# Kernel optimization log

Measured on AMD Instinct MI355X. Metric: run time of the kernel, lower is better.

## Reference

```python
import jax, jax.numpy as jnp
import numpy as np
from jax import lax

WS = 7          # window size
SHIFT = 3       # shift size
HEADS = 16
DIM = 512
NREF = 100
H_IMG = 112
W_IMG = 112
BATCH = 2
HD = DIM // HEADS
SCALE = HD ** (-0.5)
EPS = 1e-5


def _layernorm(x, w, b):
    mu = jnp.mean(x, axis=-1, keepdims=True)
    var = jnp.mean((x - mu) ** 2, axis=-1, keepdims=True)
    return (x - mu) / jnp.sqrt(var + EPS) * w + b


def _rel_pos_index():
    coords = np.stack(np.meshgrid(np.arange(WS), np.arange(WS), indexing='ij'))  # (2,ws,ws)
    cf = coords.reshape(2, -1)
    rel = cf[:, :, None] - cf[:, None, :]
    rel = rel.transpose(1, 2, 0).astype(np.int64)
    rel[..., 0] += WS - 1
    rel[..., 1] += WS - 1
    rel[..., 0] *= 2 * WS - 1
    return rel.sum(-1).reshape(-1)  # (N*N,)

_RPI = _rel_pos_index()


def setup_inputs() -> dict:
    key = jax.random.key(0)
    ks = jax.random.split(key, 16)
    C = DIM
    s = 0.02
    x = jax.random.normal(ks[0], (BATCH, H_IMG * W_IMG, C), jnp.float32)
    x_ref = jax.random.normal(ks[1], (BATCH, NREF, C), jnp.float32)
    # shifted-window attention mask (standard Swin construction)
    img = np.zeros((H_IMG, W_IMG))
    cnt = 0
    for hs in (slice(0, -WS), slice(-WS, -SHIFT), slice(-SHIFT, None)):
        for ws_ in (slice(0, -WS), slice(-WS, -SHIFT), slice(-SHIFT, None)):
            img[hs, ws_] = cnt
            cnt += 1
    mw = img.reshape(H_IMG // WS, WS, W_IMG // WS, WS).transpose(0, 2, 1, 3).reshape(-1, WS * WS)
    am = mw[:, None, :] - mw[:, :, None]
    mask = jnp.asarray(np.where(am != 0, -100.0, 0.0), jnp.float32)  # (nW, N, N)
    return dict(
        x=x, x_ref=x_ref, mask=mask,
        norm1_w=jnp.ones((C,), jnp.float32), norm1_b=jnp.zeros((C,), jnp.float32),
        qkv_w=jax.random.normal(ks[2], (3 * C, C), jnp.float32) * s,
        qkv_b=jnp.zeros((3 * C,), jnp.float32),
        diff_mu=jax.random.normal(ks[3], (1, 1, C), jnp.float32),
        diff_logsigma=jax.random.normal(ks[4], (1, 1, C), jnp.float32) * s,
        rpb_table=jax.random.normal(ks[5], ((2 * WS - 1) ** 2, HEADS), jnp.float32) * s,
        ref_qk_w=jax.random.normal(ks[6], (2 * C, C), jnp.float32) * s,
        ref_qk_b=jnp.zeros((2 * C,), jnp.float32),
        conv_w=jax.random.normal(ks[7], (HEADS, HEADS, 3, 3), jnp.float32) * s,
        conv_b=jnp.zeros((HEADS,), jnp.float32),
        proj_w=jax.random.normal(ks[8], (C, C), jnp.float32) * s,
        proj_b=jnp.zeros((C,), jnp.float32),
        norm2_w=jnp.ones((C,), jnp.float32), norm2_b=jnp.zeros((C,), jnp.float32),
        fc1_w=jax.random.normal(ks[9], (4 * C, C), jnp.float32) * s,
        fc1_b=jnp.zeros((4 * C,), jnp.float32),
        fc2_w=jax.random.normal(ks[10], (C, 4 * C), jnp.float32) * s,
        fc2_b=jnp.zeros((C,), jnp.float32),
        Hh=H_IMG, Ww=W_IMG,
    )


def _window_attention(xw, mask, x_ref, qkv_w, qkv_b, diff_mu, diff_logsigma,
                      rpb_table, ref_qk_w, ref_qk_b, conv_w, conv_b, proj_w, proj_b):
    B_, N, C = xw.shape
    rB = x_ref.shape[0]
    n_win = B_ // rB
    qkv = (xw @ qkv_w.T + qkv_b).reshape(B_, N, 3, HEADS, HD).transpose(2, 0, 3, 1, 4)
    q, k, v = qkv[0], qkv[1], qkv[2]  # (B_, heads, N, hd)
    # reference tokens -> q/v with reparameterized shift/scale
    ref_qk = (x_ref @ ref_qk_w.T + ref_qk_b).reshape(rB, NREF, 2, C).transpose(2, 0, 1, 3)
    ref_q = diff_mu + jnp.exp(diff_logsigma) * ref_qk[0]
    ref_q = ref_q.reshape(rB, NREF, HEADS, HD).transpose(0, 2, 1, 3)
    ref_v = ref_qk[1].reshape(rB, NREF, HEADS, HD).transpose(0, 2, 1, 3)
    ref_k = jnp.repeat(ref_q, n_win, axis=0)  # (B_, heads, nref, hd)
    ref_v = jnp.repeat(ref_v, n_win, axis=0)
    ra = jnp.einsum('bhnd,bhrd->bhnr', q, ref_k)  # (B_, heads, N, nref)
    ra = ra.reshape(rB, n_win, HEADS, N, NREF).transpose(0, 2, 1, 3, 4).reshape(rB, HEADS, n_win * N, NREF)
    # 3 rounds of conv diffusion + layernorm(no affine) + gelu, residual
    for _ in range(3):
        u = lax.conv_general_dilated(ra, conv_w, (1, 1), 'SAME',
                                     dimension_numbers=('NCHW', 'OIHW', 'NCHW'))
        u = u + conv_b[None, :, None, None]
        mu = jnp.mean(u, axis=(-2, -1), keepdims=True)
        var = jnp.mean((u - mu) ** 2, axis=(-2, -1), keepdims=True)
        u = jax.nn.gelu((u - mu) / jnp.sqrt(var + EPS), approximate=False)
        ra = ra + u
    ra = ra.reshape(rB, HEADS, n_win, N, NREF).transpose(0, 2, 1, 3, 4).reshape(B_, HEADS, N, NREF)
    ra = jax.nn.softmax(ra, axis=-1)
    q_new = jnp.einsum('bhnr,bhrd->bhnd', ra, ref_v) * SCALE
    attn = jnp.einsum('bhnd,bhmd->bhnm', q_new, k)
    rpb = rpb_table[_RPI].reshape(N, N, HEADS).transpose(2, 0, 1)  # (heads, N, N)
    attn = attn + rpb[None]
    nW = mask.shape[0]
    attn = attn.reshape(B_ // nW, nW, HEADS, N, N) + mask[None, :, None]
    attn = jax.nn.softmax(attn.reshape(B_, HEADS, N, N), axis=-1)
    out = jnp.einsum('bhnm,bhmd->bhnd', attn, v).transpose(0, 2, 1, 3).reshape(B_, N, C)
    return out @ proj_w.T + proj_b


def reference(x, x_ref, mask, norm1_w, norm1_b, qkv_w, qkv_b, diff_mu, diff_logsigma,
              rpb_table, ref_qk_w, ref_qk_b, conv_w, conv_b, proj_w, proj_b,
              norm2_w, norm2_b, fc1_w, fc1_b, fc2_w, fc2_b, Hh, Ww):
    B, L, C = x.shape
    shortcut = x
    xn = _layernorm(x, norm1_w, norm1_b).reshape(B, Hh, Ww, C)
    # cyclic shift
    sx = jnp.roll(xn, (-SHIFT, -SHIFT), axis=(1, 2))
    # window partition -> (B*nWin, ws*ws, C)
    xw = sx.reshape(B, Hh // WS, WS, Ww // WS, WS, C).transpose(0, 1, 3, 2, 4, 5).reshape(-1, WS * WS, C)
    aw = _window_attention(xw, mask, x_ref, qkv_w, qkv_b, diff_mu, diff_logsigma,
                           rpb_table, ref_qk_w, ref_qk_b, conv_w, conv_b, proj_w, proj_b)
    # window reverse
    sx = aw.reshape(B, Hh // WS, Ww // WS, WS, WS, C).transpose(0, 1, 3, 2, 4, 5).reshape(B, Hh, Ww, C)
    xn = jnp.roll(sx, (SHIFT, SHIFT), axis=(1, 2)).reshape(B, L, C)
    x = shortcut + xn
    h = _layernorm(x, norm2_w, norm2_b)
    h = jax.nn.gelu(h @ fc1_w.T + fc1_b, approximate=False)
    return x + (h @ fc2_w.T + fc2_b)
```

## Files before the change

### kernel.cpp

```cpp
#include <hip/hip_runtime.h>
#include <hip/hip_bf16.h>

typedef __attribute__((ext_vector_type(8))) short short8;
typedef __attribute__((ext_vector_type(8))) unsigned short ushort8;
typedef __attribute__((ext_vector_type(4))) float f32x4;
typedef __attribute__((ext_vector_type(4))) unsigned int u32x4;
typedef __attribute__((ext_vector_type(2))) unsigned int u32x2;

#define DEV __device__ __forceinline__

DEV float gelu_f(float x) { return 0.5f * x * (1.f + erff(x * 0.70710678118654752440f)); }

DEV float bf2f(unsigned short s) {
  unsigned int t = ((unsigned int)s) << 16;
  float f; __builtin_memcpy(&f, &t, 4); return f;
}
DEV unsigned short f2bf(float f) {
  __hip_bfloat16 b = __float2bfloat16(f);
  unsigned short s; __builtin_memcpy(&s, &b, 2); return s;
}

DEV void async_copy16(void* lds, const void* g) {
  __builtin_amdgcn_global_load_lds(
      (const __attribute__((address_space(1))) unsigned int*)g,
      (__attribute__((address_space(3))) unsigned int*)lds, 16, 0, 0);
}

DEV void block_reduce2(float& s, float& s2) {
  __shared__ float red[8];
  int tid = threadIdx.x;
#pragma unroll
  for (int o = 32; o > 0; o >>= 1) { s += __shfl_down(s, o); s2 += __shfl_down(s2, o); }
  if ((tid & 63) == 0) { red[tid >> 6] = s; red[4 + (tid >> 6)] = s2; }
  __syncthreads();
  s  = red[0] + red[1] + red[2] + red[3];
  s2 = red[4] + red[5] + red[6] + red[7];
}

__global__ __launch_bounds__(256) void f2b_kernel(const float* __restrict__ in,
                                                  __hip_bfloat16* __restrict__ o, int n) {
  int i = blockIdx.x * 256 + threadIdx.x;
  if (i < n) o[i] = __float2bfloat16(in[i]);
}

__global__ __launch_bounds__(256) void maskb_kernel(const float* __restrict__ mask,
                                                    unsigned short* __restrict__ maskB) {
  int i = blockIdx.x * 256 + threadIdx.x;
  int m = i % 56, rest = i / 56;
  int n = rest % 49, win = rest / 49;
  unsigned short v = 0;
  if (m < 49) v = f2bf(mask[((size_t)win * 49 + n) * 49 + m]);
  maskB[i] = v;
}

__global__ __launch_bounds__(256) void rpbt_kernel(const float* __restrict__ rpb,
                                                   unsigned short* __restrict__ rpbT) {
  int i = blockIdx.x * 256 + threadIdx.x;
  if (i >= 43904) return;
  int m = i % 56, rest = i / 56;
  int n = rest % 49, h = rest / 49;
  unsigned short v = 0;
  if (m < 49) {
    int rp = (n / 7 - m / 7 + 6) * 13 + (n % 7 - m % 7 + 6);
    v = f2bf(rpb[rp * 16 + h]);
  }
  rpbT[i] = v;
}

__global__ __launch_bounds__(256) void ln1_window_kernel(
    const float* __restrict__ x, const float* __restrict__ w, const float* __restrict__ b,
    __hip_bfloat16* __restrict__ xw) {
  int t = blockIdx.x;
  int b_ = t / 49, n = t % 49;
  int bb = b_ >> 8, win = b_ & 255;
  int wi = win >> 4, wj = win & 15;
  int ii = n / 7, jj = n % 7;
  int sh = (wi * 7 + ii + 3) % 112;
  int sw = (wj * 7 + jj + 3) % 112;
  const float* row = x + ((size_t)bb * 12544 + sh * 112 + sw) * 512;
  int tid = threadIdx.x;
  float v0 = row[tid], v1 = row[tid + 256];
  float s = v0 + v1, s2 = v0 * v0 + v1 * v1;
  block_reduce2(s, s2);
  float mu = s * (1.f / 512.f);
  float rstd = rsqrtf(s2 * (1.f / 512.f) - mu * mu + 1e-5f);
  __hip_bfloat16* orow = xw + (size_t)t * 512;
  orow[tid]       = __float2bfloat16((v0 - mu) * rstd * w[tid] + b[tid]);
  orow[tid + 256] = __float2bfloat16((v1 - mu) * rstd * w[tid + 256] + b[tid + 256]);
}

template <int EPI>
__global__ __launch_bounds__(256) void gemm_bt(
    const __hip_bfloat16* __restrict__ A, const __hip_bfloat16* __restrict__ B,
    const float* __restrict__ bias, float* __restrict__ outF,
    __hip_bfloat16* __restrict__ outB, int M, int N, int K) {
  __shared__ __align__(16) __hip_bfloat16 As[128 * 64];
  __shared__ __align__(16) __hip_bfloat16 Bs[128 * 64];
  int m0 = blockIdx.x * 128, n0 = blockIdx.y * 128;
  int tid = threadIdx.x;
  int wave = tid >> 6, lane = tid & 63;
  int wm = (wave & 1) * 64, wn = (wave >> 1) * 64;
  int lrow = lane & 15, kq = lane >> 4;
  int srow = lane >> 3, scol = (lane & 7) * 8;
  f32x4 acc[4][4] = {};
  for (int k0 = 0; k0 < K; k0 += 64) {
    int rb = wave * 32;
#pragma unroll
    for (int i = 0; i < 4; i++) {
      int row = rb + i * 8 + srow;
      async_copy16(&As[(rb + i * 8) * 64], &A[(size_t)(m0 + row) * K + k0 + scol]);
      async_copy16(&Bs[(rb + i * 8) * 64], &B[(size_t)(n0 + row) * K + k0 + scol]);
    }
    __syncthreads();
#pragma unroll
    for (int ks = 0; ks < 2; ks++) {
      short8 af[4], bf[4];
#pragma unroll
      for (int t = 0; t < 4; t++) {
        af[t] = *reinterpret_cast<const short8*>(&As[(wm + t * 16 + lrow) * 64 + ks * 32 + kq * 8]);
        bf[t] = *reinterpret_cast<const short8*>(&Bs[(wn + t * 16 + lrow) * 64 + ks * 32 + kq * 8]);
      }
#pragma unroll
      for (int tm = 0; tm < 4; tm++)
#pragma unroll
        for (int tn = 0; tn < 4; tn++)
          acc[tm][tn] = __builtin_amdgcn_mfma_f32_16x16x32_bf16(af[tm], bf[tn], acc[tm][tn], 0, 0, 0);
    }
    __syncthreads();
  }
#pragma unroll
  for (int tm = 0; tm < 4; tm++) {
#pragma unroll
    for (int tn = 0; tn < 4; tn++) {
      int col = n0 + wn + tn * 16 + lrow;
      float bv = bias[col];
#pragma unroll
      for (int r = 0; r < 4; r++) {
        int row = m0 + wm + tm * 16 + kq * 4 + r;
        float v = acc[tm][tn][r] + bv;
        size_t o = (size_t)row * N + col;
        if (EPI == 1) outB[o] = __float2bfloat16(v);
        else if (EPI == 2) outB[o] = __float2bfloat16(gelu_f(v));
        else outF[o] += v;
      }
    }
  }
}

__global__ __launch_bounds__(256) void ref_kernel(
    const float* __restrict__ x_ref, const float* __restrict__ w, const float* __restrict__ bias,
    const float* __restrict__ diff_mu, const float* __restrict__ diff_ls,
    unsigned short* __restrict__ refq, unsigned short* __restrict__ refvT) {
  int blk = blockIdx.x;
  int b = blk / 100, r = blk % 100;
  __shared__ float xs[512];
  int tid = threadIdx.x;
  const float* xr = x_ref + (size_t)(b * 100 + r) * 512;
  xs[tid] = xr[tid];
  xs[tid + 256] = xr[tid + 256];
  __syncthreads();
#pragma unroll
  for (int cc = 0; cc < 4; cc++) {
    int c = cc * 256 + tid;
    const float* wr = w + (size_t)c * 512;
    float s = bias[c];
    for (int k = 0; k < 512; k++) s += xs[k] * wr[k];
    if (c < 512) {
      float v = diff_mu[c] + expf(diff_ls[c]) * s;
      int hh = c >> 5, d = c & 31;
      refq[((size_t)(b * 16 + hh) * 100 + r) * 32 + d] = f2bf(v);
    } else {
      int c2 = c - 512, hh = c2 >> 5, d = c2 & 31;
      refvT[(((size_t)b * 16 + hh) * 32 + d) * 100 + r] = f2bf(s);
    }
  }
}

__global__ __launch_bounds__(256) void ra_kernel(
    const __hip_bfloat16* __restrict__ q, const unsigned short* __restrict__ refq,
    __hip_bfloat16* __restrict__ ra) {
  __shared__ __align__(16) unsigned short q_s[64 * 40];
  __shared__ __align__(16) unsigned short rq_s[112 * 40];
  int blk = blockIdx.x;
  int b_ = blk >> 4, h = blk & 15;
  int rb = b_ >> 8, win = b_ & 255;
  int tid = threadIdx.x;
  int wave = tid >> 6, lane = tid & 63;
  int lrow = lane & 15, kq = lane >> 4;
  u32x4 z4 = {};
  const unsigned short* qb = (const unsigned short*)q + (size_t)b_ * 49 * 512 + h * 32;
  for (int i = tid; i < 196; i += 256) {
    int n = i >> 2, c = i & 3;
    *reinterpret_cast<u32x4*>(&q_s[n * 40 + c * 8]) =
        *reinterpret_cast<const u32x4*>(&qb[n * 512 + c * 8]);
  }
  for (int i = tid; i < 60; i += 256) {
    int n = 49 + (i >> 2), c = i & 3;
    *reinterpret_cast<u32x4*>(&q_s[n * 40 + c * 8]) = z4;
  }
  const unsigned short* rqg = refq + (size_t)(rb * 16 + h) * 3200;
  for (int i = tid; i < 400; i += 256) {
    int r = i >> 2, c = i & 3;
    *reinterpret_cast<u32x4*>(&rq_s[r * 40 + c * 8]) =
        *reinterpret_cast<const u32x4*>(&rqg[r * 32 + c * 8]);
  }
  for (int i = tid; i < 48; i += 256) {
    int r = 100 + (i >> 2), c = i & 3;
    *reinterpret_cast<u32x4*>(&rq_s[r * 40 + c * 8]) = z4;
  }
  __syncthreads();
  short8 a = *reinterpret_cast<const short8*>(&q_s[(wave * 16 + lrow) * 40 + kq * 8]);
  unsigned short* ra_base = (unsigned short*)ra + ((size_t)(rb * 16 + h) * 12544 + win * 49) * 100;
  f32x4 zero = {};
#pragma unroll
  for (int nt = 0; nt < 7; nt++) {
    short8 b = *reinterpret_cast<const short8*>(&rq_s[(nt * 16 + lrow) * 40 + kq * 8]);
    f32x4 c = __builtin_amdgcn_mfma_f32_16x16x32_bf16(a, b, zero, 0, 0, 0);
    int col = nt * 16 + lrow;
#pragma unroll
    for (int r = 0; r < 4; r++) {
      int n = wave * 16 + kq * 4 + r;
      if (n < 49 && col < 100) ra_base[n * 100 + col] = f2bf(c[r]);
    }
  }
}

__global__ __launch_bounds__(256) void conv_kernel(
    const __hip_bfloat16* __restrict__ ra_, const float* __restrict__ cw, const float* __restrict__ cb,
    __hip_bfloat16* __restrict__ u_, float* __restrict__ psum, float* __restrict__ psumsq) {
  __shared__ __align__(16) unsigned short in_s[6 * 103 * 24];
  __shared__ __align__(16) unsigned short w_s[16 * 160];
  __shared__ float sred_s[4][16], sred_s2[4][16];
  const unsigned short* ra = (const unsigned short*)ra_;
  unsigned short* u = (unsigned short*)u_;
  int yt = blockIdx.x, bb = blockIdx.y;
  int y0 = yt * 4;
  int tid = threadIdx.x;
  int wave = tid >> 6, lane = tid & 63;
  int lrow = lane & 15, kq = lane >> 4;
  for (int i = tid; i < 2560; i += 256) {
    int co = i / 160, k = i % 160;
    unsigned short v = 0;
    if (k < 144) {
      int ci = k & 15, p = k >> 4;
      v = f2bf(cw[(co * 16 + ci) * 9 + p]);
    }
    w_s[i] = v;
  }
  for (int i = tid; i < 288; i += 256) {
    int ci = i & 15, rem = i >> 4;
    int yl = rem / 3, xs = rem % 3;
    int xl = (xs == 0) ? 0 : (100 + xs);
    in_s[(yl * 103 + xl) * 24 + ci] = 0;
  }
  if (tid < 192) {
    int unit = tid >> 1, par = tid & 1;
    int ci = unit / 6, yl = unit % 6;
    int gy = y0 - 1 + yl;
    bool rv = (gy >= 0 && gy < 12544);
    const unsigned short* rp = ra + (((size_t)bb * 16 + ci) * 12544 + (rv ? gy : 0)) * 100;
    unsigned short* lp = &in_s[(yl * 103 + 1) * 24 + ci];
#pragma unroll 4
    for (int c = par; c < 25; c += 2) {
      u32x2 d = {0u, 0u};
      if (rv) d = *reinterpret_cast<const u32x2*>(&rp[c * 4]);
      lp[(c * 4 + 0) * 24] = (unsigned short)(d[0] & 0xffff);
      lp[(c * 4 + 1) * 24] = (unsigned short)(d[0] >> 16);
      lp[(c * 4 + 2) * 24] = (unsigned short)(d[1] & 0xffff);
      lp[(c * 4 + 3) * 24] = (unsigned short)(d[1] >> 16);
    }
  }
  __syncthreads();

  short8 afr[5];
#pragma unroll
  for (int c = 0; c < 5; c++)
    afr[c] = *reinterpret_cast<const short8*>(&w_s[lrow * 160 + c * 32 + kq * 8]);
  int kqh = kq >> 1, ci0 = (kq & 1) * 8;
  int kyA[5], kxA[5];
#pragma unroll
  for (int c = 0; c < 5; c++) {
    int p = c * 2 + kqh; if (p > 8) p = 0;
    kyA[c] = p / 3; kxA[c] = p % 3;
  }
  float bias_r[4];
#pragma unroll
  for (int r = 0; r < 4; r++) bias_r[r] = cb[kq * 4 + r];
  float s_r[4] = {0.f, 0.f, 0.f, 0.f}, s2_r[4] = {0.f, 0.f, 0.f, 0.f};

  int yl = wave;
  int gy = y0 + yl;
#pragma unroll
  for (int xg = 0; xg < 7; xg++) {
    int px = xg * 16 + lrow;
    int pxc = px < 100 ? px : 99;
    f32x4 acc = {};
#pragma unroll
    for (int c = 0; c < 5; c++) {
      short8 bfrag = *reinterpret_cast<const short8*>(
          &in_s[((yl + kyA[c]) * 103 + pxc + kxA[c]) * 24 + ci0]);
      acc = __builtin_amdgcn_mfma_f32_16x16x32_bf16(afr[c], bfrag, acc, 0, 0, 0);
    }
    bool valid = px < 100;
#pragma unroll
    for (int r = 0; r < 4; r++) {
      float v = acc[r] + bias_r[r];
      if (valid) {
        u[(((size_t)bb * 16 + kq * 4 + r) * 12544 + gy) * 100 + px] = f2bf(v);
        s_r[r] += v; s2_r[r] += v * v;
      }
    }
  }
#pragma unroll
  for (int o = 1; o < 16; o <<= 1)
#pragma unroll
    for (int r = 0; r < 4; r++) { s_r[r] += __shfl_xor(s_r[r], o); s2_r[r] += __shfl_xor(s2_r[r], o); }
  if (lrow == 0)
#pragma unroll
    for (int r = 0; r < 4; r++) { sred_s[wave][kq * 4 + r] = s_r[r]; sred_s2[wave][kq * 4 + r] = s2_r[r]; }
  __syncthreads();
  if (tid < 16) {
    float s  = sred_s[0][tid] + sred_s[1][tid] + sred_s[2][tid] + sred_s[3][tid];
    float s2 = sred_s2[0][tid] + sred_s2[1][tid] + sred_s2[2][tid] + sred_s2[3][tid];
    size_t pi = ((size_t)bb * 3136 + yt) * 16 + tid;
    psum[pi] = s; psumsq[pi] = s2;
  }
}

__global__ __launch_bounds__(256) void conv_stats_kernel(
    const float* __restrict__ psum, const float* __restrict__ psumsq, float* __restrict__ stats) {
  int g = blockIdx.x;
  int bb = g >> 4, co = g & 15;
  int tid = threadIdx.x;
  float s = 0.f, s2 = 0.f;
  for (int t = tid; t < 3136; t += 256) {
    size_t pi = ((size_t)bb * 3136 + t) * 16 + co;
    s += psum[pi];
    s2 += psumsq[pi];
  }
  block_reduce2(s, s2);
  if (tid == 0) {
    const float inv = 1.f / 1254400.f;
    float mu = s * inv;
    float var = s2 * inv - mu * mu;
    stats[g * 2] = mu;
    stats[g * 2 + 1] = rsqrtf(var + 1e-5f);
  }
}

__global__ __launch_bounds__(256) void conv_apply_kernel(
    __hip_bfloat16* __restrict__ ra, const __hip_bfloat16* __restrict__ u,
    const float* __restrict__ stats) {
  const int total8 = 5017600;
  int stride = gridDim.x * 256;
  for (int i = blockIdx.x * 256 + threadIdx.x; i < total8; i += stride) {
    int g = i / 156800;
    float mu = stats[g * 2], rstd = stats[g * 2 + 1];
    ushort8 uu = reinterpret_cast<const ushort8*>(u)[i];
    ushort8 rr = reinterpret_cast<const ushort8*>(ra)[i];
    ushort8 oo;
#pragma unroll
    for (int j = 0; j < 8; j++) {
      float rv = bf2f(rr[j]) + gelu_f((bf2f(uu[j]) - mu) * rstd);
      oo[j] = f2bf(rv);
    }
    reinterpret_cast<ushort8*>(ra)[i] = oo;
  }
}

template <int FUSE>
__global__ __launch_bounds__(256) void attn_kernel(
    const __hip_bfloat16* __restrict__ ra_, const __hip_bfloat16* __restrict__ u_,
    const float* __restrict__ stats, const unsigned short* __restrict__ refvT,
    const __hip_bfloat16* __restrict__ kv_, const unsigned short* __restrict__ rpbT,
    const unsigned short* __restrict__ maskB, __hip_bfloat16* __restrict__ att_) {
  __shared__ __align__(16) char smem[36608];
  unsigned short* P1  = (unsigned short*)smem;
  unsigned short* rvT = (unsigned short*)(smem + 17408);
  unsigned short* P2  = (unsigned short*)smem;
  unsigned short* vT  = (unsigned short*)(smem + 9216);
  unsigned short* qn  = (unsigned short*)(smem + 26112);
  unsigned short* kb  = (unsigned short*)(smem + 31232);
  float* lsum         = (float*)(smem + 36352);

  int blk = blockIdx.x;
  int b_ = blk >> 4, h = blk & 15;
  int rb = b_ >> 8, win = b_ & 255;
  int tid = threadIdx.x;
  int wave = tid >> 6, lane = tid & 63;
  int lrow = lane & 15, kq = lane >> 4;
  const unsigned short* ra = (const unsigned short*)ra_;
  const unsigned short* ug = (const unsigned short*)u_;
  const unsigned short* kv = (const unsigned short*)kv_;
  unsigned short* att = (unsigned short*)att_;
  u32x2 zz = {};

  if (tid < 64) lsum[tid] = 1.0f;
  float mu = 0.f, rstd = 0.f;
  if (FUSE) { mu = stats[(rb * 16 + h) * 2]; rstd = stats[(rb * 16 + h) * 2 + 1]; }

  const size_t tile_off = ((size_t)(rb * 16 + h) * 12544 + win * 49) * 100;
  const unsigned short* rab = ra + tile_off;
  const unsigned short* uab = ug + tile_off;
  for (int i = tid; i < 1225; i += 256) {
    int n = i / 25, c = i % 25;
    u32x2 rv = *reinterpret_cast<const u32x2*>(&rab[n * 100 + c * 4]);
    if (FUSE) {
      u32x2 uv = *reinterpret_cast<const u32x2*>(&uab[n * 100 + c * 4]);
      unsigned short rr4[4] = {(unsigned short)(rv[0] & 0xffff), (unsigned short)(rv[0] >> 16),
                               (unsigned short)(rv[1] & 0xffff), (unsigned short)(rv[1] >> 16)};
      unsigned short uu4[4] = {(unsigned short)(uv[0] & 0xffff), (unsigned short)(uv[0] >> 16),
                               (unsigned short)(uv[1] & 0xffff), (unsigned short)(uv[1] >> 16)};
      unsigned short o4[4];
#pragma unroll
      for (int j = 0; j < 4; j++)
        o4[j] = f2bf(bf2f(rr4[j]) + gelu_f((bf2f(uu4[j]) - mu) * rstd));
      u32x2 w;
      w[0] = (unsigned int)o4[0] | ((unsigned int)o4[1] << 16);
      w[1] = (unsigned int)o4[2] | ((unsigned int)o4[3] << 16);
      *reinterpret_cast<u32x2*>(&P1[n * 136 + c * 4]) = w;
    } else {
      *reinterpret_cast<u32x2*>(&P1[n * 136 + c * 4]) = rv;
    }
  }
  for (int i = tid; i < 343; i += 256) {
    int n = i / 7, c = i % 7;
    *reinterpret_cast<u32x2*>(&P1[n * 136 + 100 + c * 4]) = zz;
  }
  const unsigned short* rvtg = refvT + (size_t)(rb * 16 + h) * 3200;
  for (int i = tid; i < 800; i += 256) {
    int d = i / 25, c = i % 25;
    *reinterpret_cast<u32x2*>(&rvT[d * 136 + c * 4]) =
        *reinterpret_cast<const u32x2*>(&rvtg[d * 100 + c * 4]);
  }
  for (int i = tid; i < 224; i += 256) {
    int d = i / 7, c = i % 7;
    *reinterpret_cast<u32x2*>(&rvT[d * 136 + 100 + c * 4]) = zz;
  }
  const unsigned short* kvb = kv + (size_t)b_ * 49 * 1024;
  for (int i = tid; i < 196; i += 256) {
    int m = i >> 2, c = i & 3;
    *reinterpret_cast<u32x4*>(&kb[m * 40 + c * 8]) =
        *reinterpret_cast<const u32x4*>(&kvb[m * 1024 + h * 32 + c * 8]);
  }
  __syncthreads();

  if (tid < 196) {
    int n = tid >> 2, q = tid & 3;
    unsigned short* row = P1 + n * 136 + q * 25;
    float e[25];
#pragma unroll
    for (int r = 0; r < 25; r++) e[r] = bf2f(row[r]);
    float mx = -1e30f;
#pragma unroll
    for (int r = 0; r < 25; r++) mx = fmaxf(mx, e[r]);
    mx = fmaxf(mx, __shfl_xor(mx, 1));
    mx = fmaxf(mx, __shfl_xor(mx, 2));
    float sm = 0.f;
#pragma unroll
    for (int r = 0; r < 25; r++) { e[r] = __expf(e[r] - mx); sm += e[r]; }
    sm += __shfl_xor(sm, 1);
    sm += __shfl_xor(sm, 2);
#pragma unroll
    for (int r = 0; r < 25; r++) row[r] = f2bf(e[r]);
    if (q == 0) lsum[n] = sm;
  }
  __syncthreads();

  f32x4 acc1[2] = {};
#pragma unroll
  for (int ks = 0; ks < 4; ks++) {
    short8 a = *reinterpret_cast<const short8*>(&P1[(wave * 16 + lrow) * 136 + ks * 32 + kq * 8]);
#pragma unroll
    for (int dt = 0; dt < 2; dt++) {
      short8 b = *reinterpret_cast<const short8*>(&rvT[(dt * 16 + lrow) * 136 + ks * 32 + kq * 8]);
      acc1[dt] = __builtin_amdgcn_mfma_f32_16x16x32_bf16(a, b, acc1[dt], 0, 0, 0);
    }
  }
  float invl[4];
#pragma unroll
  for (int r = 0; r < 4; r++)
    invl[r] = 0.17677669529663688f / lsum[wave * 16 + kq * 4 + r];
#pragma unroll
  for (int dt = 0; dt < 2; dt++)
#pragma unroll
    for (int r = 0; r < 4; r++) {
      int n = wave * 16 + kq * 4 + r;
      qn[n * 40 + dt * 16 + lrow] = f2bf(acc1[dt][r] * invl[r]);
    }
  __syncthreads();

  for (int i = tid; i < 196; i += 256) {
    int m = i >> 2, dg = (i & 3) * 8;
    ushort8 vv = *reinterpret_cast<const ushort8*>(&kvb[m * 1024 + 512 + h * 32 + dg]);
#pragma unroll
    for (int j = 0; j < 8; j++) vT[(dg + j) * 72 + m] = vv[j];
  }
  for (int i = tid; i < 480; i += 256) vT[(i / 15) * 72 + 49 + i % 15] = 0;

  const unsigned short* bt = maskB + (size_t)win * 2744;
  const unsigned short* rt = rpbT + (size_t)h * 2744;
  short8 aq = *reinterpret_cast<const short8*>(&qn[(wave * 16 + lrow) * 40 + kq * 8]);
  f32x4 zero = {};
  float val[4][4];
#pragma unroll
  for (int mt = 0; mt < 4; mt++) {
    short8 bk = *reinterpret_cast<const short8*>(&kb[(mt * 16 + lrow) * 40 + kq * 8]);
    f32x4 lg = __builtin_amdgcn_mfma_f32_16x16x32_bf16(aq, bk, zero, 0, 0, 0);
    int m = mt * 16 + lrow;
#pragma unroll
    for (int r = 0; r < 4; r++) {
      int n = wave * 16 + kq * 4 + r;
      float v;
      if (m < 49 && n < 49)
        v = lg[r] + bf2f(rt[n * 56 + m]) + bf2f(bt[n * 56 + m]);
      else v = -1e30f;
      val[mt][r] = v;
    }
  }
#pragma unroll
  for (int r = 0; r < 4; r++) {
    float mx = -1e30f;
#pragma unroll
    for (int mt = 0; mt < 4; mt++) mx = fmaxf(mx, val[mt][r]);
    mx = fmaxf(mx, __shfl_xor(mx, 1)); mx = fmaxf(mx, __shfl_xor(mx, 2));
    mx = fmaxf(mx, __shfl_xor(mx, 4)); mx = fmaxf(mx, __shfl_xor(mx, 8));
    float sm = 0.f, e[4];
#pragma unroll
    for (int mt = 0; mt < 4; mt++) { e[mt] = __expf(val[mt][r] - mx); sm += e[mt]; }
    sm += __shfl_xor(sm, 1); sm += __shfl_xor(sm, 2);
    sm += __shfl_xor(sm, 4); sm += __shfl_xor(sm, 8);
    float inv = 1.f / sm;
    int n = wave * 16 + kq * 4 + r;
#pragma unroll
    for (int mt = 0; mt < 4; mt++) P2[n * 72 + mt * 16 + lrow] = f2bf(e[mt] * inv);
  }
  __syncthreads();

  f32x4 acc2[2] = {};
#pragma unroll
  for (int ks = 0; ks < 2; ks++) {
    short8 ap = *reinterpret_cast<const short8*>(&P2[(wave * 16 + lrow) * 72 + ks * 32 + kq * 8]);
#pragma unroll
    for (int dt = 0; dt < 2; dt++) {
      short8 bv = *reinterpret_cast<const short8*>(&vT[(dt * 16 + lrow) * 72 + ks * 32 + kq * 8]);
      acc2[dt] = __builtin_amdgcn_mfma_f32_16x16x32_bf16(ap, bv, acc2[dt], 0, 0, 0);
    }
  }
  unsigned short* ab = att + (size_t)b_ * 49 * 512 + h * 32;
#pragma unroll
  for (int dt = 0; dt < 2; dt++)
#pragma unroll
    for (int r = 0; r < 4; r++) {
      int n = wave * 16 + kq * 4 + r;
      if (n < 49) ab[n * 512 + dt * 16 + lrow] = f2bf(acc2[dt][r]);
    }
}

__global__ __launch_bounds__(256) void resid_ln2_kernel(
    const float* __restrict__ x, const __hip_bfloat16* __restrict__ proj_out,
    const float* __restrict__ w2, const float* __restrict__ b2,
    float* __restrict__ out, __hip_bfloat16* __restrict__ hout) {
  int blk = blockIdx.x;
  int bb = blk / 12544, l = blk % 12544;
  int hh = l / 112, ww = l % 112;
  int hs = (hh + 109) % 112, wsx = (ww + 109) % 112;
  int t = (bb * 256 + (hs / 7) * 16 + (wsx / 7)) * 49 + (hs % 7) * 7 + (wsx % 7);
  const float* xr = x + (size_t)blk * 512;
  const __hip_bfloat16* pr = proj_out + (size_t)t * 512;
  int tid = threadIdx.x;
  float v0 = xr[tid] + __bfloat162float(pr[tid]);
  float v1 = xr[tid + 256] + __bfloat162float(pr[tid + 256]);
  float* orow = out + (size_t)blk * 512;
  orow[tid] = v0;
  orow[tid + 256] = v1;
  float s = v0 + v1, s2 = v0 * v0 + v1 * v1;
  block_reduce2(s, s2);
  float mu = s * (1.f / 512.f);
  float rstd = rsqrtf(s2 * (1.f / 512.f) - mu * mu + 1e-5f);
  __hip_bfloat16* hrow = hout + (size_t)blk * 512;
  hrow[tid]       = __float2bfloat16((v0 - mu) * rstd * w2[tid] + b2[tid]);
  hrow[tid + 256] = __float2bfloat16((v1 - mu) * rstd * w2[tid + 256] + b2[tid + 256]);
}

extern "C" void kernel_launch(void* const* d_in, const int* in_sizes, int n_in,
                              void* d_out, int out_size, void* d_ws, size_t ws_size,
                              hipStream_t stream) {
  const float* x       = (const float*)d_in[0];
  const float* x_ref   = (const float*)d_in[1];
  const float* mask    = (const float*)d_in[2];
  const float* n1w     = (const float*)d_in[3];
  const float* n1b     = (const float*)d_in[4];
  const float* qkv_w   = (const float*)d_in[5];
  const float* qkv_b   = (const float*)d_in[6];
  const float* diff_mu = (const float*)d_in[7];
  const float* diff_ls = (const float*)d_in[8];
  const float* rpb     = (const float*)d_in[9];
  const float* ref_w   = (const float*)d_in[10];
  const float* ref_b   = (const float*)d_in[11];
  const float* conv_w  = (const float*)d_in[12];
  const float* conv_b  = (const float*)d_in[13];
  const float* proj_w  = (const float*)d_in[14];
  const float* proj_b  = (const float*)d_in[15];
  const float* n2w     = (const float*)d_in[16];
  const float* n2b     = (const float*)d_in[17];
  const float* fc1_w   = (const float*)d_in[18];
  const float* fc1_b   = (const float*)d_in[19];
  const float* fc2_w   = (const float*)d_in[20];
  const float* fc2_b   = (const float*)d_in[21];
  float* out = (float*)d_out;

  char* ws = (char*)d_ws;
  size_t off = 0;
  auto alloc = [&](size_t bytes) -> char* {
    char* p = ws + off;
    off += (bytes + 255) & ~(size_t)255;
    return p;
  };
  __hip_bfloat16* wq_bf = (__hip_bfloat16*)alloc(1536ULL * 512 * 2);
  __hip_bfloat16* wp_bf = (__hip_bfloat16*)alloc(512ULL * 512 * 2);
  __hip_bfloat16* w1_bf = (__hip_bfloat16*)alloc(2048ULL * 512 * 2);
  __hip_bfloat16* w2_bf = (__hip_bfloat16*)alloc(512ULL * 2048 * 2);
  unsigned short* refq  = (unsigned short*)alloc(2ULL * 16 * 100 * 32 * 2);
  unsigned short* refvT = (unsigned short*)alloc(2ULL * 16 * 32 * 100 * 2);
  unsigned short* maskB = (unsigned short*)alloc(256ULL * 49 * 56 * 2);
  unsigned short* rpbT  = (unsigned short*)alloc(16ULL * 49 * 56 * 2);
  float* psum  = (float*)alloc(2ULL * 3136 * 16 * 4);
  float* psumq = (float*)alloc(2ULL * 3136 * 16 * 4);
  float* stats = (float*)alloc(64 * 4);
  char* regX  = alloc(25088ULL * 512 * 2);
  char* regQ  = alloc(25088ULL * 512 * 2);
  char* regRA = alloc(2ULL * 16 * 12544 * 100 * 2);
  char* regU  = alloc(2ULL * 16 * 12544 * 100 * 2);

  __hip_bfloat16* xw_bf   = (__hip_bfloat16*)regX;
  __hip_bfloat16* att_bf  = (__hip_bfloat16*)regX;
  __hip_bfloat16* q_bf    = (__hip_bfloat16*)regQ;
  __hip_bfloat16* h_bf    = (__hip_bfloat16*)regQ;
  __hip_bfloat16* ra      = (__hip_bfloat16*)regRA;
  __hip_bfloat16* hg      = (__hip_bfloat16*)regRA;
  __hip_bfloat16* u       = (__hip_bfloat16*)regU;
  __hip_bfloat16* proj_bf = (__hip_bfloat16*)(regU + 51380224);

  const size_t kv_bytes = 25088ULL * 1024 * 2;
  bool fused = (ws_size >= off + kv_bytes);
  __hip_bfloat16* kv_bf = fused ? (__hip_bfloat16*)alloc(kv_bytes)
                                : (__hip_bfloat16*)regU;

  f2b_kernel<<<3072, 256, 0, stream>>>(qkv_w, wq_bf, 786432);
  f2b_kernel<<<1024, 256, 0, stream>>>(proj_w, wp_bf, 262144);
  f2b_kernel<<<4096, 256, 0, stream>>>(fc1_w, w1_bf, 1048576);
  f2b_kernel<<<4096, 256, 0, stream>>>(fc2_w, w2_bf, 1048576);
  maskb_kernel<<<2744, 256, 0, stream>>>(mask, maskB);
  rpbt_kernel<<<172, 256, 0, stream>>>(rpb, rpbT);
  ln1_window_kernel<<<25088, 256, 0, stream>>>(x, n1w, n1b, xw_bf);
  gemm_bt<1><<<dim3(196, 4), 256, 0, stream>>>(xw_bf, wq_bf, qkv_b, nullptr, q_bf,
                                               25088, 512, 512);
  ref_kernel<<<200, 256, 0, stream>>>(x_ref, ref_w, ref_b, diff_mu, diff_ls, refq, refvT);
  ra_kernel<<<8192, 256, 0, stream>>>(q_bf, refq, ra);
  for (int rd = 0; rd < 3; rd++) {
    conv_kernel<<<dim3(3136, 2), 256, 0, stream>>>(ra, conv_w, conv_b, u, psum, psumq);
    conv_stats_kernel<<<32, 256, 0, stream>>>(psum, psumq, stats);
    if (rd < 2 || !fused)
      conv_apply_kernel<<<4096, 256, 0, stream>>>(ra, u, stats);
  }
  gemm_bt<1><<<dim3(196, 8), 256, 0, stream>>>(xw_bf, wq_bf + 512 * 512, qkv_b + 512,
                                               nullptr, kv_bf, 25088, 1024, 512);
  if (fused)
    attn_kernel<1><<<8192, 256, 0, stream>>>(ra, u, stats, refvT, kv_bf, rpbT, maskB, att_bf);
  else
    attn_kernel<0><<<8192, 256, 0, stream>>>(ra, u, stats, refvT, kv_bf, rpbT, maskB, att_bf);
  gemm_bt<1><<<dim3(196, 4), 256, 0, stream>>>(att_bf, wp_bf, proj_b, nullptr, proj_bf,
                                               25088, 512, 512);
  resid_ln2_kernel<<<25088, 256, 0, stream>>>(x, proj_bf, n2w, n2b, out, h_bf);
  for (int ch = 0; ch < 2; ch++) {
    const __hip_bfloat16* hA = h_bf + (size_t)ch * 12544 * 512;
    gemm_bt<2><<<dim3(98, 16), 256, 0, stream>>>(hA, w1_bf, fc1_b, nullptr, hg,
                                                 12544, 2048, 512);
    gemm_bt<3><<<dim3(98, 4), 256, 0, stream>>>(hg, w2_bf, fc2_b,
                                                out + (size_t)ch * 12544 * 512, nullptr,
                                                12544, 512, 2048);
  }
}
```

Before: 1.186 ms.

## Use wave-per-row layernorms and shrink attention LDS by reordering phases

The two layernorm kernels (LN1 with window gather, and residual+LN2) now process one row per wavefront, using 16-byte vector loads and stores and a shuffle-only reduction instead of a block-wide reduction, with four times fewer blocks. The attention kernel's shared memory drops from about 36.6KB to 27KB. It does this by running softmax and the ref-value MFMA before loading K, reusing the freed region for K, and storing the row sums in the qn padding. The aim is fewer barriers and less per-block work in the layernorms and more resident attention blocks per CU. The price is an extra __syncthreads and tighter aliasing between LDS regions in the attention kernel.

Measured after the change: 1.160 ms. 1.02x faster.

```diff
diff --git a/kernel.cpp b/kernel.cpp
--- a/kernel.cpp
+++ b/kernel.cpp
@@ -70,7 +70,9 @@
 __global__ __launch_bounds__(256) void ln1_window_kernel(
     const float* __restrict__ x, const float* __restrict__ w, const float* __restrict__ b,
     __hip_bfloat16* __restrict__ xw) {
-  int t = blockIdx.x;
+  int tid = threadIdx.x;
+  int wave = tid >> 6, lane = tid & 63;
+  int t = blockIdx.x * 4 + wave;
   int b_ = t / 49, n = t % 49;
   int bb = b_ >> 8, win = b_ & 255;
   int wi = win >> 4, wj = win & 15;
@@ -78,15 +80,29 @@
   int sh = (wi * 7 + ii + 3) % 112;
   int sw = (wj * 7 + jj + 3) % 112;
   const float* row = x + ((size_t)bb * 12544 + sh * 112 + sw) * 512;
-  int tid = threadIdx.x;
-  float v0 = row[tid], v1 = row[tid + 256];
-  float s = v0 + v1, s2 = v0 * v0 + v1 * v1;
-  block_reduce2(s, s2);
+  f32x4 v0 = *reinterpret_cast<const f32x4*>(&row[lane * 8]);
+  f32x4 v1 = *reinterpret_cast<const f32x4*>(&row[lane * 8 + 4]);
+  float s = 0.f, s2 = 0.f;
+#pragma unroll
+  for (int j = 0; j < 4; j++) {
+    s += v0[j] + v1[j];
+    s2 += v0[j] * v0[j] + v1[j] * v1[j];
+  }
+#pragma unroll
+  for (int o = 1; o < 64; o <<= 1) { s += __shfl_xor(s, o); s2 += __shfl_xor(s2, o); }
   float mu = s * (1.f / 512.f);
   float rstd = rsqrtf(s2 * (1.f / 512.f) - mu * mu + 1e-5f);
-  __hip_bfloat16* orow = xw + (size_t)t * 512;
-  orow[tid]       = __float2bfloat16((v0 - mu) * rstd * w[tid] + b[tid]);
-  orow[tid + 256] = __float2bfloat16((v1 - mu) * rstd * w[tid + 256] + b[tid + 256]);
+  f32x4 w0 = *reinterpret_cast<const f32x4*>(&w[lane * 8]);
+  f32x4 w1 = *reinterpret_cast<const f32x4*>(&w[lane * 8 + 4]);
+  f32x4 c0 = *reinterpret_cast<const f32x4*>(&b[lane * 8]);
+  f32x4 c1 = *reinterpret_cast<const f32x4*>(&b[lane * 8 + 4]);
+  ushort8 o8;
+#pragma unroll
+  for (int j = 0; j < 4; j++) {
+    o8[j]     = f2bf((v0[j] - mu) * rstd * w0[j] + c0[j]);
+    o8[4 + j] = f2bf((v1[j] - mu) * rstd * w1[j] + c1[j]);
+  }
+  *reinterpret_cast<ushort8*>((unsigned short*)xw + (size_t)t * 512 + lane * 8) = o8;
 }
 
 template <int EPI>
@@ -374,14 +390,15 @@
     const float* __restrict__ stats, const unsigned short* __restrict__ refvT,
     const __hip_bfloat16* __restrict__ kv_, const unsigned short* __restrict__ rpbT,
     const unsigned short* __restrict__ maskB, __hip_bfloat16* __restrict__ att_) {
-  __shared__ __align__(16) char smem[36608];
+  __shared__ __align__(16) char smem[27136];
   unsigned short* P1  = (unsigned short*)smem;
-  unsigned short* rvT = (unsigned short*)(smem + 17408);
+  unsigned short* rvT = (unsigned short*)(smem + 13312);
+  unsigned short* qn  = (unsigned short*)(smem + 22016);
   unsigned short* P2  = (unsigned short*)smem;
   unsigned short* vT  = (unsigned short*)(smem + 9216);
-  unsigned short* qn  = (unsigned short*)(smem + 26112);
-  unsigned short* kb  = (unsigned short*)(smem + 31232);
-  float* lsum         = (float*)(smem + 36352);
+  unsigned short* kb  = (unsigned short*)(smem + 13824);
+
+#define LSUM(n) (*reinterpret_cast<float*>(&qn[(n) * 40 + 32]))
 
   int blk = blockIdx.x;
   int b_ = blk >> 4, h = blk & 15;
@@ -395,7 +412,7 @@
   unsigned short* att = (unsigned short*)att_;
   u32x2 zz = {};
 
-  if (tid < 64) lsum[tid] = 1.0f;
+  if (tid < 64) LSUM(tid) = 1.0f;
   float mu = 0.f, rstd = 0.f;
   if (FUSE) { mu = stats[(rb * 16 + h) * 2]; rstd = stats[(rb * 16 + h) * 2 + 1]; }
 
@@ -437,59 +454,59 @@
     int d = i / 7, c = i % 7;
     *reinterpret_cast<u32x2*>(&rvT[d * 136 + 100 + c * 4]) = zz;
   }
+  __syncthreads();
+
+  if (tid < 196) {
+    int n = tid >> 2, q = tid & 3;
+    unsigned short* row = P1 + n * 136 + q * 25;
+    float e[25];
+#pragma unroll
+    for (int r = 0; r < 25; r++) e[r] = bf2f(row[r]);
+    float mx = -1e30f;
+#pragma unroll
+    for (int r = 0; r < 25; r++) mx = fmaxf(mx, e[r]);
+    mx = fmaxf(mx, __shfl_xor(mx, 1));
+    mx = fmaxf(mx, __shfl_xor(mx, 2));
+    float sm = 0.f;
+#pragma unroll
+    for (int r = 0; r < 25; r++) { e[r] = __expf(e[r] - mx); sm += e[r]; }
+    sm += __shfl_xor(sm, 1);
+    sm += __shfl_xor(sm, 2);
+#pragma unroll
+    for (int r = 0; r < 25; r++) row[r] = f2bf(e[r]);
+    if (q == 0) LSUM(n) = sm;
+  }
+  __syncthreads();
+
+  f32x4 acc1[2] = {};
+#pragma unroll
+  for (int ks = 0; ks < 4; ks++) {
+    short8 a = *reinterpret_cast<const short8*>(&P1[(wave * 16 + lrow) * 136 + ks * 32 + kq * 8]);
+#pragma unroll
+    for (int dt = 0; dt < 2; dt++) {
+      short8 b = *reinterpret_cast<const short8*>(&rvT[(dt * 16 + lrow) * 136 + ks * 32 + kq * 8]);
+      acc1[dt] = __builtin_amdgcn_mfma_f32_16x16x32_bf16(a, b, acc1[dt], 0, 0, 0);
+    }
+  }
+  float invl[4];
+#pragma unroll
+  for (int r = 0; r < 4; r++)
+    invl[r] = 0.17677669529663688f / LSUM(wave * 16 + kq * 4 + r);
+#pragma unroll
+  for (int dt = 0; dt < 2; dt++)
+#pragma unroll
+    for (int r = 0; r < 4; r++) {
+      int n = wave * 16 + kq * 4 + r;
+      qn[n * 40 + dt * 16 + lrow] = f2bf(acc1[dt][r] * invl[r]);
+    }
+  __syncthreads();
+
   const unsigned short* kvb = kv + (size_t)b_ * 49 * 1024;
   for (int i = tid; i < 196; i += 256) {
     int m = i >> 2, c = i & 3;
     *reinterpret_cast<u32x4*>(&kb[m * 40 + c * 8]) =
         *reinterpret_cast<const u32x4*>(&kvb[m * 1024 + h * 32 + c * 8]);
   }
-  __syncthreads();
-
-  if (tid < 196) {
-    int n = tid >> 2, q = tid & 3;
-    unsigned short* row = P1 + n * 136 + q * 25;
-    float e[25];
-#pragma unroll
-    for (int r = 0; r < 25; r++) e[r] = bf2f(row[r]);
-    float mx = -1e30f;
-#pragma unroll
-    for (int r = 0; r < 25; r++) mx = fmaxf(mx, e[r]);
-    mx = fmaxf(mx, __shfl_xor(mx, 1));
-    mx = fmaxf(mx, __shfl_xor(mx, 2));
-    float sm = 0.f;
-#pragma unroll
-    for (int r = 0; r < 25; r++) { e[r] = __expf(e[r] - mx); sm += e[r]; }
-    sm += __shfl_xor(sm, 1);
-    sm += __shfl_xor(sm, 2);
-#pragma unroll
-    for (int r = 0; r < 25; r++) row[r] = f2bf(e[r]);
-    if (q == 0) lsum[n] = sm;
-  }
-  __syncthreads();
-
-  f32x4 acc1[2] = {};
-#pragma unroll
-  for (int ks = 0; ks < 4; ks++) {
-    short8 a = *reinterpret_cast<const short8*>(&P1[(wave * 16 + lrow) * 136 + ks * 32 + kq * 8]);
-#pragma unroll
-    for (int dt = 0; dt < 2; dt++) {
-      short8 b = *reinterpret_cast<const short8*>(&rvT[(dt * 16 + lrow) * 136 + ks * 32 + kq * 8]);
-      acc1[dt] = __builtin_amdgcn_mfma_f32_16x16x32_bf16(a, b, acc1[dt], 0, 0, 0);
-    }
-  }
-  float invl[4];
-#pragma unroll
-  for (int r = 0; r < 4; r++)
-    invl[r] = 0.17677669529663688f / lsum[wave * 16 + kq * 4 + r];
-#pragma unroll
-  for (int dt = 0; dt < 2; dt++)
-#pragma unroll
-    for (int r = 0; r < 4; r++) {
-      int n = wave * 16 + kq * 4 + r;
-      qn[n * 40 + dt * 16 + lrow] = f2bf(acc1[dt][r] * invl[r]);
-    }
-  __syncthreads();
-
   for (int i = tid; i < 196; i += 256) {
     int m = i >> 2, dg = (i & 3) * 8;
     ushort8 vv = *reinterpret_cast<const ushort8*>(&kvb[m * 1024 + 512 + h * 32 + dg]);
@@ -497,6 +514,7 @@
     for (int j = 0; j < 8; j++) vT[(dg + j) * 72 + m] = vv[j];
   }
   for (int i = tid; i < 480; i += 256) vT[(i / 15) * 72 + 49 + i % 15] = 0;
+  __syncthreads();
 
   const unsigned short* bt = maskB + (size_t)win * 2744;
   const unsigned short* rt = rpbT + (size_t)h * 2744;
@@ -555,32 +573,55 @@
       int n = wave * 16 + kq * 4 + r;
       if (n < 49) ab[n * 512 + dt * 16 + lrow] = f2bf(acc2[dt][r]);
     }
+#undef LSUM
 }
 
 __global__ __launch_bounds__(256) void resid_ln2_kernel(
     const float* __restrict__ x, const __hip_bfloat16* __restrict__ proj_out,
     const float* __restrict__ w2, const float* __restrict__ b2,
     float* __restrict__ out, __hip_bfloat16* __restrict__ hout) {
-  int blk = blockIdx.x;
+  int tid = threadIdx.x;
+  int wave = tid >> 6, lane = tid & 63;
+  int blk = blockIdx.x * 4 + wave;
   int bb = blk / 12544, l = blk % 12544;
   int hh = l / 112, ww = l % 112;
   int hs = (hh + 109) % 112, wsx = (ww + 109) % 112;
   int t = (bb * 256 + (hs / 7) * 16 + (wsx / 7)) * 49 + (hs % 7) * 7 + (wsx % 7);
-  const float* xr = x + (size_t)blk * 512;
-  const __hip_bfloat16* pr = proj_out + (size_t)t * 512;
-  int tid = threadIdx.x;
-  float v0 = xr[tid] + __bfloat162float(pr[tid]);
-  float v1 = xr[tid + 256] + __bfloat162float(pr[tid + 256]);
-  float* orow = out + (size_t)blk * 512;
-  orow[tid] = v0;
-  orow[tid + 256] = v1;
-  float s = v0 + v1, s2 = v0 * v0 + v1 * v1;
-  block_reduce2(s, s2);
+  const float* xr = x + (size_t)blk * 512 + lane * 8;
+  const unsigned short* pr = (const unsigned short*)proj_out + (size_t)t * 512 + lane * 8;
+  f32x4 x0 = *reinterpret_cast<const f32x4*>(xr);
+  f32x4 x1 = *reinterpret_cast<const f32x4*>(xr + 4);
+  ushort8 p8 = *reinterpret_cast<const ushort8*>(pr);
+  float v[8];
+#pragma unroll
+  for (int j = 0; j < 4; j++) {
+    v[j]     = x0[j] + bf2f(p8[j]);
+    v[4 + j] = x1[j] + bf2f(p8[4 + j]);
+  }
+  float s = 0.f, s2 = 0.f;
+#pragma unroll
+  for (int j = 0; j < 8; j++) { s += v[j]; s2 += v[j] * v[j]; }
+  float* orow = out + (size_t)blk * 512 + lane * 8;
+  f32x4 o0, o1;
+#pragma unroll
+  for (int j = 0; j < 4; j++) { o0[j] = v[j]; o1[j] = v[4 + j]; }
+  *reinterpret_cast<f32x4*>(orow) = o0;
+  *reinterpret_cast<f32x4*>(orow + 4) = o1;
+#pragma unroll
+  for (int o = 1; o < 64; o <<= 1) { s += __shfl_xor(s, o); s2 += __shfl_xor(s2, o); }
   float mu = s * (1.f / 512.f);
   float rstd = rsqrtf(s2 * (1.f / 512.f) - mu * mu + 1e-5f);
-  __hip_bfloat16* hrow = hout + (size_t)blk * 512;
-  hrow[tid]       = __float2bfloat16((v0 - mu) * rstd * w2[tid] + b2[tid]);
-  hrow[tid + 256] = __float2bfloat16((v1 - mu) * rstd * w2[tid + 256] + b2[tid + 256]);
+  f32x4 w0 = *reinterpret_cast<const f32x4*>(&w2[lane * 8]);
+  f32x4 w1 = *reinterpret_cast<const f32x4*>(&w2[lane * 8 + 4]);
+  f32x4 c0 = *reinterpret_cast<const f32x4*>(&b2[lane * 8]);
+  f32x4 c1 = *reinterpret_cast<const f32x4*>(&b2[lane * 8 + 4]);
+  ushort8 h8;
+#pragma unroll
+  for (int j = 0; j < 4; j++) {
+    h8[j]     = f2bf((v[j] - mu) * rstd * w0[j] + c0[j]);
+    h8[4 + j] = f2bf((v[4 + j] - mu) * rstd * w1[j] + c1[j]);
+  }
+  *reinterpret_cast<ushort8*>((unsigned short*)hout + (size_t)blk * 512 + lane * 8) = h8;
 }
 
 extern "C" void kernel_launch(void* const* d_in, const int* in_sizes, int n_in,
@@ -653,7 +694,7 @@
   f2b_kernel<<<4096, 256, 0, stream>>>(fc2_w, w2_bf, 1048576);
   maskb_kernel<<<2744, 256, 0, stream>>>(mask, maskB);
   rpbt_kernel<<<172, 256, 0, stream>>>(rpb, rpbT);
-  ln1_window_kernel<<<25088, 256, 0, stream>>>(x, n1w, n1b, xw_bf);
+  ln1_window_kernel<<<6272, 256, 0, stream>>>(x, n1w, n1b, xw_bf);
   gemm_bt<1><<<dim3(196, 4), 256, 0, stream>>>(xw_bf, wq_bf, qkv_b, nullptr, q_bf,
                                                25088, 512, 512);
   ref_kernel<<<200, 256, 0, stream>>>(x_ref, ref_w, ref_b, diff_mu, diff_ls, refq, refvT);
@@ -672,7 +713,7 @@
     attn_kernel<0><<<8192, 256, 0, stream>>>(ra, u, stats, refvT, kv_bf, rpbT, maskB, att_bf);
   gemm_bt<1><<<dim3(196, 4), 256, 0, stream>>>(att_bf, wp_bf, proj_b, nullptr, proj_bf,
                                                25088, 512, 512);
-  resid_ln2_kernel<<<25088, 256, 0, stream>>>(x, proj_bf, n2w, n2b, out, h_bf);
+  resid_ln2_kernel<<<6272, 256, 0, stream>>>(x, proj_bf, n2w, n2b, out, h_bf);
   for (int ch = 0; ch < 2; ch++) {
     const __hip_bfloat16* hA = h_bf + (size_t)ch * 12544 * 512;
     gemm_bt<2><<<dim3(98, 16), 256, 0, stream>>>(hA, w1_bf, fc1_b, nullptr, hg,
```
